# Kernel tuning notes

Measured on AMD Instinct MI355X. Metric: run time of the kernel, lower is better.

The kernel has to match this reference:

```python
import jax, jax.numpy as jnp
import numpy as np

B, L, E = 64, 256, 256
H, M, HD, R, O = 512, 256, 64, 4, 1024
CI = E + R * HD          # controller input size = 512
TO = H + R * HD          # pre-output size = 768
EPS = 1e-5


def _ln(x, g, b):
    m = jnp.mean(x, axis=-1, keepdims=True)
    v = jnp.mean((x - m) ** 2, axis=-1, keepdims=True)
    return (x - m) * jax.lax.rsqrt(v + EPS) * g + b


def setup_inputs() -> dict:
    key = jax.random.key(0)
    ks = jax.random.split(key, 12)
    s = 0.02
    return {
        "x_emb": jax.random.normal(ks[0], (B, L, E), jnp.float32),
        "W_ih": jax.random.normal(ks[1], (4 * H, CI), jnp.float32) * s,
        "W_hh": jax.random.normal(ks[2], (4 * H, H), jnp.float32) * s,
        "b_ih": jnp.zeros((4 * H,), jnp.float32),
        "b_hh": jnp.zeros((4 * H,), jnp.float32),
        "ln_in_g": jnp.ones((CI,), jnp.float32), "ln_in_b": jnp.zeros((CI,), jnp.float32),
        "ln_h_g": jnp.ones((H,), jnp.float32), "ln_h_b": jnp.zeros((H,), jnp.float32),
        "W_rk": jax.random.normal(ks[3], (R * HD, H), jnp.float32) * s, "b_rk": jnp.zeros((R * HD,), jnp.float32),
        "W_wk": jax.random.normal(ks[4], (HD, H), jnp.float32) * s, "b_wk": jnp.zeros((HD,), jnp.float32),
        "W_ws": jax.random.normal(ks[5], (1, H), jnp.float32) * s, "b_ws": jnp.zeros((1,), jnp.float32),
        "W_er": jax.random.normal(ks[6], (HD, H), jnp.float32) * s, "b_er": jnp.zeros((HD,), jnp.float32),
        "W_ad": jax.random.normal(ks[7], (HD, H), jnp.float32) * s, "b_ad": jnp.zeros((HD,), jnp.float32),
        "ln_rk_g": jnp.ones((HD,), jnp.float32), "ln_rk_b": jnp.zeros((HD,), jnp.float32),
        "ln_wk_g": jnp.ones((HD,), jnp.float32), "ln_wk_b": jnp.zeros((HD,), jnp.float32),
        "ln_mem_g": jnp.ones((HD,), jnp.float32), "ln_mem_b": jnp.zeros((HD,), jnp.float32),
        "ln_out_g": jnp.ones((TO,), jnp.float32), "ln_out_b": jnp.zeros((TO,), jnp.float32),
        "W_proj": jax.random.normal(ks[8], (O, TO), jnp.float32) * s, "b_proj": jnp.zeros((O,), jnp.float32),
    }


def reference(x_emb, W_ih, W_hh, b_ih, b_hh, ln_in_g, ln_in_b, ln_h_g, ln_h_b,
              W_rk, b_rk, W_wk, b_wk, W_ws, b_ws, W_er, b_er, W_ad, b_ad,
              ln_rk_g, ln_rk_b, ln_wk_g, ln_wk_b, ln_mem_g, ln_mem_b,
              ln_out_g, ln_out_b, W_proj, b_proj):
    Bd = x_emb.shape[0]

    def step(carry, x_t):
        h, c, memory, read_vec = carry
        ci = _ln(jnp.concatenate([x_t, read_vec], axis=-1), ln_in_g, ln_in_b)
        # single-step LSTM (PyTorch gate order i, f, g, o)
        gates = ci @ W_ih.T + h @ W_hh.T + b_ih + b_hh
        i, f, g, o = jnp.split(gates, 4, axis=-1)
        c = jax.nn.sigmoid(f) * c + jax.nn.sigmoid(i) * jnp.tanh(g)
        h = jax.nn.sigmoid(o) * jnp.tanh(c)
        hn = _ln(h, ln_h_g, ln_h_b)
        read_keys = (hn @ W_rk.T + b_rk).reshape(Bd, R, HD)
        write_keys = hn @ W_wk.T + b_wk                       # [B, HD]
        write_str = jax.nn.sigmoid(hn @ W_ws.T + b_ws)        # [B, 1]
        erase_vec = jax.nn.sigmoid(hn @ W_er.T + b_er)        # [B, HD]
        write_vec = jnp.tanh(hn @ W_ad.T + b_ad)              # [B, HD]
        # write
        mem_n = _ln(memory, ln_mem_g, ln_mem_b)
        wk = _ln(write_keys, ln_wk_g, ln_wk_b)
        ww = jax.nn.softmax(jnp.einsum('bh,bmh->bm', wk, mem_n), axis=1) * write_str  # [B, M]
        memory = memory * (1.0 - ww[:, :, None] * erase_vec[:, None, :]) + ww[:, :, None] * write_vec[:, None, :]
        # read
        mem_n2 = _ln(memory, ln_mem_g, ln_mem_b)
        rk = _ln(read_keys, ln_rk_g, ln_rk_b)
        rw = jax.nn.softmax(jnp.einsum('bnh,bmh->bnm', rk, mem_n2), axis=2)
        read_vec = jnp.einsum('bnm,bmh->bnh', rw, memory).reshape(Bd, R * HD)
        out = _ln(jnp.concatenate([hn, read_vec], axis=-1), ln_out_g, ln_out_b)
        logits = out @ W_proj.T + b_proj
        return (h, c, memory, read_vec), logits

    h0 = jnp.zeros((Bd, H), x_emb.dtype)
    c0 = jnp.zeros((Bd, H), x_emb.dtype)
    mem0 = jnp.zeros((Bd, M, HD), x_emb.dtype)
    rv0 = jnp.zeros((Bd, R * HD), x_emb.dtype)
    (h, c, memory, _), ys = jax.lax.scan(step, (h0, c0, mem0, rv0), jnp.swapaxes(x_emb, 0, 1))
    outputs = jnp.swapaxes(ys, 0, 1)  # [B, L, O]
    return outputs, memory, (h[None], c[None])
```

## Files before the change

kernel.cpp:

```cpp
#include <hip/hip_runtime.h>
#include <stdint.h>

#define Bn 64
#define Ln 256
#define En 256
#define Hn 512
#define Mn 256
#define HDn 64
#define Rn 4
#define On 1024
#define CIn 512
#define TOn 768
#define TB 1024
#define MP 65

typedef __attribute__((ext_vector_type(2))) _Float16 h2_t;

__device__ __forceinline__ float dot2(uint32_t a, uint32_t b, float c) {
  return __builtin_amdgcn_fdot2(__builtin_bit_cast(h2_t, a),
                                __builtin_bit_cast(h2_t, b), c, false);
}
__device__ __forceinline__ uint32_t pk2(float a, float b) {
  h2_t h; h.x = (_Float16)a; h.y = (_Float16)b;
  return __builtin_bit_cast(uint32_t, h);
}
__device__ __forceinline__ float sigm(float x) {
  float e = __expf(-fabsf(x)); float s = 1.0f / (1.0f + e);
  return x >= 0.0f ? s : 1.0f - s;
}
__device__ __forceinline__ float tanh_(float x) {
  float e = __expf(-2.0f * fabsf(x)); float t = (1.0f - e) / (1.0f + e);
  return x >= 0.0f ? t : -t;
}
__device__ __forceinline__ float ln64(float v, float g, float b) {
  float s = v;
  #pragma unroll
  for (int o = 32; o; o >>= 1) s += __shfl_xor(s, o);
  float mean = s * (1.f / 64.f);
  float d = v - mean; float q = d * d;
  #pragma unroll
  for (int o = 32; o; o >>= 1) q += __shfl_xor(q, o);
  float rstd = rsqrtf(q * (1.f / 64.f) + 1e-5f);
  return d * rstd * g + b;
}

__global__ void pack_gates4(const float* __restrict__ W_ih,
                            const float* __restrict__ W_hh,
                            uint4* __restrict__ Wg4) {
  int idx = blockIdx.x * 256 + threadIdx.x;
  if (idx >= 512 * 512) return;
  int kk = idx >> 9, u = idx & 511;
  int c = 2 * kk;
  float v[8];
  #pragma unroll
  for (int r = 0; r < 4; r++) {
    int row = r * 512 + u;
    float a, bb;
    if (c < 512) { a = W_ih[row * 512 + c];        bb = W_ih[row * 512 + c + 1]; }
    else         { a = W_hh[row * 512 + (c - 512)]; bb = W_hh[row * 512 + (c - 512) + 1]; }
    v[2 * r] = a; v[2 * r + 1] = bb;
  }
  uint4 w; w.x = pk2(v[0], v[1]); w.y = pk2(v[2], v[3]);
  w.z = pk2(v[4], v[5]); w.w = pk2(v[6], v[7]);
  Wg4[(size_t)kk * 512 + u] = w;
}

__global__ void pack_heads4(const float* __restrict__ W_rk, const float* __restrict__ W_wk,
                            const float* __restrict__ W_ws, const float* __restrict__ W_er,
                            const float* __restrict__ W_ad, uint4* __restrict__ Whd4) {
  int idx = blockIdx.x * 256 + threadIdx.x;
  if (idx >= 256 * 128) return;
  int kk = idx >> 7, s4 = idx & 127;
  int c = 2 * kk;
  float v[8];
  #pragma unroll
  for (int j = 0; j < 4; j++) {
    int s = 4 * s4 + j;
    float a = 0.f, bb = 0.f;
    if (s < 256)      { a = W_rk[s * 512 + c];          bb = W_rk[s * 512 + c + 1]; }
    else if (s < 320) { a = W_wk[(s - 256) * 512 + c];  bb = W_wk[(s - 256) * 512 + c + 1]; }
    else if (s == 320){ a = W_ws[c];                    bb = W_ws[c + 1]; }
    else if (s < 385) { a = W_er[(s - 321) * 512 + c];  bb = W_er[(s - 321) * 512 + c + 1]; }
    else if (s < 449) { a = W_ad[(s - 385) * 512 + c];  bb = W_ad[(s - 385) * 512 + c + 1]; }
    v[2 * j] = a; v[2 * j + 1] = bb;
  }
  uint4 w; w.x = pk2(v[0], v[1]); w.y = pk2(v[2], v[3]);
  w.z = pk2(v[4], v[5]); w.w = pk2(v[6], v[7]);
  Whd4[(size_t)kk * 128 + s4] = w;
}

__global__ void pack_proj(const float* __restrict__ W_proj, uint32_t* __restrict__ Wp) {
  int idx = blockIdx.x * blockDim.x + threadIdx.x;
  if (idx >= 1024 * 384) return;
  int o = idx / 384, kk = idx - o * 384;
  int c = 2 * kk;
  Wp[(size_t)kk * 1024 + o] = pk2(W_proj[o * 768 + c], W_proj[o * 768 + c + 1]);
}

struct Params {
  const float *x, *b_ih, *b_hh;
  const float *ln_in_g, *ln_in_b, *ln_h_g, *ln_h_b;
  const float *b_rk, *b_wk, *b_ws, *b_er, *b_ad;
  const float *ln_rk_g, *ln_rk_b, *ln_wk_g, *ln_wk_b;
  const float *ln_mem_g, *ln_mem_b, *ln_out_g, *ln_out_b;
  const uint4* Wg4; const uint4* Whd4;
  uint32_t* out16; float* out;
};

#define SMEM_FLOATS 32736
#define SMEM_BYTES  (SMEM_FLOATS * 4)

__global__ __launch_bounds__(TB, 1) void dnc_recur(Params p) {
  extern __shared__ float smem[];
  float* mem  = smem;
  float* h32  = mem + 16640;
  float* c32  = h32 + 512;
  float* hn32 = c32 + 512;
  float* rv32 = hn32 + 512;
  float* cvec = rv32 + 256;
  float* hd   = cvec + 512;
  float* wkn  = hd + 512;
  float* rkn  = wkn + 64;
  float* erv  = rkn + 256;
  float* wvv  = erv + 64;
  float* wsc  = wvv + 64;
  float* rsc  = wsc + 256;
  float* redA = rsc + 1024;
  float* redB = redA + 32;
  float* redC = redB + 32;
  float* redD = redC + 16;
  float* redE = redD + 32;
  float* misc = redE + 32;
  float* gpart= misc + 16;
  float* Lin_g= gpart + 4096;
  float* Lin_b= Lin_g + 512;
  float* Lh_g = Lin_b + 512;
  float* Lh_b = Lh_g + 512;
  float* Lo_g = Lh_b + 512;
  float* Lo_b = Lo_g + 768;
  float* Lrk_g= Lo_b + 768;
  float* Lrk_b= Lrk_g + 64;
  float* Lwk_g= Lrk_b + 64;
  float* Lwk_b= Lwk_g + 64;
  float* Lm_g = Lwk_b + 64;
  float* Lm_b = Lm_g + 64;
  float* bsum = Lm_b + 64;
  float* bhd  = bsum + 2048;
  uint32_t* act16 = (uint32_t*)(bhd + 512);
  uint32_t* hn16  = act16 + 512;

  const int tid = threadIdx.x;
  const int b = blockIdx.x;

  for (int i = tid; i < 16640; i += TB) mem[i] = 0.f;
  if (tid < 512) {
    h32[tid] = 0.f; c32[tid] = 0.f;
    Lin_g[tid] = p.ln_in_g[tid]; Lin_b[tid] = p.ln_in_b[tid];
    Lh_g[tid]  = p.ln_h_g[tid];  Lh_b[tid]  = p.ln_h_b[tid];
    float4 bs;
    bs.x = p.b_ih[tid]        + p.b_hh[tid];
    bs.y = p.b_ih[512 + tid]  + p.b_hh[512 + tid];
    bs.z = p.b_ih[1024 + tid] + p.b_hh[1024 + tid];
    bs.w = p.b_ih[1536 + tid] + p.b_hh[1536 + tid];
    ((float4*)bsum)[tid] = bs;
    float bb = 0.f;
    if (tid < 256)       bb = p.b_rk[tid];
    else if (tid < 320)  bb = p.b_wk[tid - 256];
    else if (tid == 320) bb = p.b_ws[0];
    else if (tid < 385)  bb = p.b_er[tid - 321];
    else if (tid < 449)  bb = p.b_ad[tid - 385];
    bhd[tid] = bb;
  }
  if (tid < 768) { Lo_g[tid] = p.ln_out_g[tid]; Lo_b[tid] = p.ln_out_b[tid]; }
  if (tid < 64) {
    Lrk_g[tid] = p.ln_rk_g[tid]; Lrk_b[tid] = p.ln_rk_b[tid];
    Lwk_g[tid] = p.ln_wk_g[tid]; Lwk_b[tid] = p.ln_wk_b[tid];
    Lm_g[tid]  = p.ln_mem_g[tid]; Lm_b[tid] = p.ln_mem_b[tid];
  }
  if (tid < 256) { rv32[tid] = 0.f; act16[256 + tid] = 0u; }
  __syncthreads();

  for (int t = 0; t < Ln; ++t) {
    if (tid < 256)      cvec[tid] = p.x[((size_t)b * Ln + t) * En + tid];
    else if (tid < 512) cvec[tid] = rv32[tid - 256];
    __syncthreads();
    {
      float v = (tid < 512) ? cvec[tid] : 0.f;
      float s = v, q = v * v;
      #pragma unroll
      for (int o = 32; o; o >>= 1) { s += __shfl_xor(s, o); q += __shfl_xor(q, o); }
      if ((tid & 63) == 0) { redA[tid >> 6] = s; redA[16 + (tid >> 6)] = q; }
    }
    __syncthreads();
    {
      float s = 0.f, q = 0.f;
      #pragma unroll
      for (int i = 0; i < 16; i++) { s += redA[i]; q += redA[16 + i]; }
      float mean = s * (1.f / 512.f);
      float rstd = rsqrtf(q * (1.f / 512.f) - mean * mean + 1e-5f);
      if (tid < 256) {
        float v0 = (cvec[2 * tid]     - mean) * rstd * Lin_g[2 * tid]     + Lin_b[2 * tid];
        float v1 = (cvec[2 * tid + 1] - mean) * rstd * Lin_g[2 * tid + 1] + Lin_b[2 * tid + 1];
        act16[tid] = pk2(v0, v1);
      }
    }
    __syncthreads();

    {
      int u = tid & 511, kh = tid >> 9;
      const uint4* wp = p.Wg4 + (size_t)(kh * 256) * 512 + u;
      const uint32_t* ap = act16 + kh * 256;
      float a0 = 0.f, a1 = 0.f, a2 = 0.f, a3 = 0.f;
      uint4 Ab[8], Bb[8];
      #pragma unroll
      for (int j = 0; j < 8; j++) Ab[j] = wp[(size_t)j * 512];
      #pragma unroll 1
      for (int c = 0; c < 32; c += 2) {
        #pragma unroll
        for (int j = 0; j < 8; j++) Bb[j] = wp[(size_t)((c + 1) * 8 + j) * 512];
        #pragma unroll
        for (int j = 0; j < 8; j++) {
          uint32_t a = ap[c * 8 + j];
          a0 = dot2(Ab[j].x, a, a0); a1 = dot2(Ab[j].y, a, a1);
          a2 = dot2(Ab[j].z, a, a2); a3 = dot2(Ab[j].w, a, a3);
        }
        int cn = (c + 2) & 31;
        #pragma unroll
        for (int j = 0; j < 8; j++) Ab[j] = wp[(size_t)(cn * 8 + j) * 512];
        #pragma unroll
        for (int j = 0; j < 8; j++) {
          uint32_t a = ap[(c + 1) * 8 + j];
          a0 = dot2(Bb[j].x, a, a0); a1 = dot2(Bb[j].y, a, a1);
          a2 = dot2(Bb[j].z, a, a2); a3 = dot2(Bb[j].w, a, a3);
        }
      }
      float4 r; r.x = a0; r.y = a1; r.z = a2; r.w = a3;
      ((float4*)(gpart + kh * 2048))[u] = r;
    }
    __syncthreads();

    if (tid < 512) {
      float4 pa = ((float4*)gpart)[tid];
      float4 pb = ((float4*)gpart)[512 + tid];
      float4 bs = ((float4*)bsum)[tid];
      float gi = pa.x + pb.x + bs.x;
      float gf = pa.y + pb.y + bs.y;
      float gg = pa.z + pb.z + bs.z;
      float go = pa.w + pb.w + bs.w;
      float c_ = sigm(gf) * c32[tid] + sigm(gi) * tanh_(gg);
      float h_ = sigm(go) * tanh_(c_);
      c32[tid] = c_; h32[tid] = h_;
    }
    __syncthreads();
    {
      float v = (tid < 512) ? h32[tid] : 0.f;
      float s = v, q = v * v;
      #pragma unroll
      for (int o = 32; o; o >>= 1) { s += __shfl_xor(s, o); q += __shfl_xor(q, o); }
      if ((tid & 63) == 0) { redB[tid >> 6] = s; redB[16 + (tid >> 6)] = q; }
    }
    __syncthreads();
    {
      float s = 0.f, q = 0.f;
      #pragma unroll
      for (int i = 0; i < 16; i++) { s += redB[i]; q += redB[16 + i]; }
      float mean = s * (1.f / Hn);
      float rstd = rsqrtf(q * (1.f / Hn) - mean * mean + 1e-5f);
      if (tid < 512) hn32[tid] = (h32[tid] - mean) * rstd * Lh_g[tid] + Lh_b[tid];
      if (tid < 256) {
        float v0 = (h32[2 * tid]     - mean) * rstd * Lh_g[2 * tid]     + Lh_b[2 * tid];
        float v1 = (h32[2 * tid + 1] - mean) * rstd * Lh_g[2 * tid + 1] + Lh_b[2 * tid + 1];
        hn16[tid] = pk2(v0, v1);
        act16[256 + tid] = pk2(h32[2 * tid], h32[2 * tid + 1]);
      }
    }
    __syncthreads();

    {
      int s4 = tid & 127, kp = tid >> 7;
      const uint4* wp = p.Whd4 + (size_t)(kp * 32) * 128 + s4;
      const uint32_t* ap = hn16 + kp * 32;
      float a0 = 0.f, a1 = 0.f, a2 = 0.f, a3 = 0.f;
      uint4 Ab[8], Bb[8];
      #pragma unroll
      for (int j = 0; j < 8; j++) Ab[j] = wp[(size_t)j * 128];
      #pragma unroll 1
      for (int c = 0; c < 4; c += 2) {
        #pragma unroll
        for (int j = 0; j < 8; j++) Bb[j] = wp[(size_t)((c + 1) * 8 + j) * 128];
        #pragma unroll
        for (int j = 0; j < 8; j++) {
          uint32_t a = ap[c * 8 + j];
          a0 = dot2(Ab[j].x, a, a0); a1 = dot2(Ab[j].y, a, a1);
          a2 = dot2(Ab[j].z, a, a2); a3 = dot2(Ab[j].w, a, a3);
        }
        int cn = (c + 2) & 3;
        #pragma unroll
        for (int j = 0; j < 8; j++) Ab[j] = wp[(size_t)(cn * 8 + j) * 128];
        #pragma unroll
        for (int j = 0; j < 8; j++) {
          uint32_t a = ap[(c + 1) * 8 + j];
          a0 = dot2(Bb[j].x, a, a0); a1 = dot2(Bb[j].y, a, a1);
          a2 = dot2(Bb[j].z, a, a2); a3 = dot2(Bb[j].w, a, a3);
        }
      }
      float4 r; r.x = a0; r.y = a1; r.z = a2; r.w = a3;
      ((float4*)(gpart + kp * 512))[s4] = r;
    }
    __syncthreads();
    if (tid < 512) {
      float acc = bhd[tid];
      #pragma unroll
      for (int kp = 0; kp < 8; kp++) acc += gpart[kp * 512 + tid];
      hd[tid] = acc;
    }
    __syncthreads();

    {
      int wid = tid >> 6, lane = tid & 63;
      if (wid == 0) {
        wkn[lane] = ln64(hd[256 + lane], Lwk_g[lane], Lwk_b[lane]);
      } else if (wid <= 4) {
        int n = wid - 1;
        rkn[n * 64 + lane] = ln64(hd[n * 64 + lane], Lrk_g[lane], Lrk_b[lane]);
      } else if (wid == 5) {
        erv[lane] = sigm(hd[321 + lane]);
      } else if (wid == 6) {
        wvv[lane] = tanh_(hd[385 + lane]);
      } else if (wid == 7 && lane == 0) {
        misc[0] = sigm(hd[320]);
      }
    }
    __syncthreads();

    {
      int m = tid >> 2, q = tid & 3;
      const float* mrow = mem + m * MP + q * 16;
      float s1 = 0.f, s2 = 0.f;
      #pragma unroll
      for (int j = 0; j < 16; j++) { float v = mrow[j]; s1 += v; s2 += v * v; }
      s1 += __shfl_xor(s1, 1); s1 += __shfl_xor(s1, 2);
      s2 += __shfl_xor(s2, 1); s2 += __shfl_xor(s2, 2);
      float mean = s1 * (1.f / 64.f);
      float rstd = rsqrtf(s2 * (1.f / 64.f) - mean * mean + 1e-5f);
      float d = 0.f;
      #pragma unroll
      for (int j = 0; j < 16; j++) {
        int jj = q * 16 + j;
        float mn = (mrow[j] - mean) * rstd * Lm_g[jj] + Lm_b[jj];
        d += wkn[jj] * mn;
      }
      d += __shfl_xor(d, 1); d += __shfl_xor(d, 2);
      if (q == 0) wsc[m] = d;
    }
    __syncthreads();
    float wsv = 0.f;
    if (tid < 256) {
      wsv = wsc[tid];
      float mx = wsv;
      #pragma unroll
      for (int o = 32; o; o >>= 1) mx = fmaxf(mx, __shfl_xor(mx, o));
      float e = __expf(wsv - mx);
      float sm = e;
      #pragma unroll
      for (int o = 32; o; o >>= 1) sm += __shfl_xor(sm, o);
      if ((tid & 63) == 0) { redC[tid >> 6] = mx; redC[8 + (tid >> 6)] = sm; }
    }
    __syncthreads();
    if (tid < 256) {
      float M = fmaxf(fmaxf(redC[0], redC[1]), fmaxf(redC[2], redC[3]));
      float S = redC[8]  * __expf(redC[0] - M) + redC[9]  * __expf(redC[1] - M)
              + redC[10] * __expf(redC[2] - M) + redC[11] * __expf(redC[3] - M);
      wsc[tid] = __expf(wsv - M) / S * misc[0];
    }
    __syncthreads();

    {
      int m = tid >> 2, q = tid & 3;
      float w = wsc[m];
      float* mrow = mem + m * MP + q * 16;
      float vals[16];
      float s1 = 0.f, s2 = 0.f;
      #pragma unroll
      for (int j = 0; j < 16; j++) {
        int jj = q * 16 + j;
        float v = mrow[j];
        v = v * (1.f - w * erv[jj]) + w * wvv[jj];
        mrow[j] = v;
        vals[j] = v;
        s1 += v; s2 += v * v;
      }
      s1 += __shfl_xor(s1, 1); s1 += __shfl_xor(s1, 2);
      s2 += __shfl_xor(s2, 1); s2 += __shfl_xor(s2, 2);
      float mean = s1 * (1.f / 64.f);
      float rstd = rsqrtf(s2 * (1.f / 64.f) - mean * mean + 1e-5f);
      float d0 = 0.f, d1 = 0.f, d2 = 0.f, d3 = 0.f;
      #pragma unroll
      for (int j = 0; j < 16; j++) {
        int jj = q * 16 + j;
        float mn = (vals[j] - mean) * rstd * Lm_g[jj] + Lm_b[jj];
        d0 += rkn[jj] * mn;       d1 += rkn[64 + jj] * mn;
        d2 += rkn[128 + jj] * mn; d3 += rkn[192 + jj] * mn;
      }
      d0 += __shfl_xor(d0, 1); d0 += __shfl_xor(d0, 2);
      d1 += __shfl_xor(d1, 1); d1 += __shfl_xor(d1, 2);
      d2 += __shfl_xor(d2, 1); d2 += __shfl_xor(d2, 2);
      d3 += __shfl_xor(d3, 1); d3 += __shfl_xor(d3, 2);
      if (q == 0) { rsc[m] = d0; rsc[256 + m] = d1; rsc[512 + m] = d2; rsc[768 + m] = d3; }
    }
    __syncthreads();
    float rsv;
    {
      int w = tid >> 6;
      rsv = rsc[tid];
      float mx = rsv;
      #pragma unroll
      for (int o = 32; o; o >>= 1) mx = fmaxf(mx, __shfl_xor(mx, o));
      float e = __expf(rsv - mx);
      float sm = e;
      #pragma unroll
      for (int o = 32; o; o >>= 1) sm += __shfl_xor(sm, o);
      if ((tid & 63) == 0) { redD[w] = mx; redD[16 + w] = sm; }
    }
    __syncthreads();
    {
      int n = tid >> 8;
      float M = fmaxf(fmaxf(redD[4 * n], redD[4 * n + 1]),
                      fmaxf(redD[4 * n + 2], redD[4 * n + 3]));
      float S = redD[16 + 4 * n]     * __expf(redD[4 * n]     - M)
              + redD[16 + 4 * n + 1] * __expf(redD[4 * n + 1] - M)
              + redD[16 + 4 * n + 2] * __expf(redD[4 * n + 2] - M)
              + redD[16 + 4 * n + 3] * __expf(redD[4 * n + 3] - M);
      rsc[tid] = __expf(rsv - M) / S;
    }
    __syncthreads();

    {
      int out = tid >> 2, q = tid & 3;
      int n = out >> 6, j = out & 63;
      const float* rw = rsc + n * 256 + q * 64;
      float acc = 0.f;
      #pragma unroll 8
      for (int mm = 0; mm < 64; ++mm)
        acc += rw[mm] * mem[(q * 64 + mm) * MP + j];
      acc += __shfl_xor(acc, 1); acc += __shfl_xor(acc, 2);
      if (q == 0) rv32[out] = acc;
    }
    __syncthreads();

    {
      float v = (tid < 512) ? hn32[tid] : (tid < 768 ? rv32[tid - 512] : 0.f);
      float s = v, q = v * v;
      #pragma unroll
      for (int o = 32; o; o >>= 1) { s += __shfl_xor(s, o); q += __shfl_xor(q, o); }
      if ((tid & 63) == 0) { redE[tid >> 6] = s; redE[16 + (tid >> 6)] = q; }
    }
    __syncthreads();
    {
      float s = 0.f, q = 0.f;
      #pragma unroll
      for (int i = 0; i < 16; i++) { s += redE[i]; q += redE[16 + i]; }
      float mean = s * (1.f / TOn);
      float rstd = rsqrtf(q * (1.f / TOn) - mean * mean + 1e-5f);
      if (tid < 384) {
        int e0 = 2 * tid, e1 = e0 + 1;
        float u0 = (e0 < 512) ? hn32[e0] : rv32[e0 - 512];
        float u1 = (e1 < 512) ? hn32[e1] : rv32[e1 - 512];
        u0 = (u0 - mean) * rstd * Lo_g[e0] + Lo_b[e0];
        u1 = (u1 - mean) * rstd * Lo_g[e1] + Lo_b[e1];
        p.out16[((size_t)b * Ln + t) * 384 + tid] = pk2(u0, u1);
      }
    }
  }

  const size_t OUT0 = (size_t)Bn * Ln * On;
  const size_t OUT1 = OUT0 + (size_t)Bn * Mn * HDn;
  const size_t OUT2 = OUT1 + (size_t)Bn * Hn;
  for (int i = tid; i < Mn * HDn; i += TB)
    p.out[OUT0 + (size_t)b * Mn * HDn + i] = mem[(i >> 6) * MP + (i & 63)];
  if (tid < Hn) {
    p.out[OUT1 + (size_t)b * Hn + tid] = h32[tid];
    p.out[OUT2 + (size_t)b * Hn + tid] = c32[tid];
  }
}

#define PROJ_ROWS 32
__global__ __launch_bounds__(1024, 1) void proj_gemm(const uint32_t* __restrict__ out16,
                                                     const uint32_t* __restrict__ Wp,
                                                     const float* __restrict__ b_proj,
                                                     float* __restrict__ out) {
  __shared__ uint32_t arow[PROJ_ROWS][384];
  int r0 = blockIdx.x * PROJ_ROWS;
  int tid = threadIdx.x;
  for (int i = tid; i < PROJ_ROWS * 384; i += 1024)
    ((uint32_t*)arow)[i] = out16[(size_t)r0 * 384 + i];
  __syncthreads();
  int cq = tid & 255, rg = tid >> 8;
  float acc[8][4];
  #pragma unroll
  for (int i = 0; i < 8; i++)
    #pragma unroll
    for (int j = 0; j < 4; j++) acc[i][j] = 0.f;
  for (int kk = 0; kk < 384; ++kk) {
    uint32_t w0 = Wp[(size_t)kk * 1024 + cq];
    uint32_t w1 = Wp[(size_t)kk * 1024 + cq + 256];
    uint32_t w2 = Wp[(size_t)kk * 1024 + cq + 512];
    uint32_t w3 = Wp[(size_t)kk * 1024 + cq + 768];
    #pragma unroll
    for (int i = 0; i < 8; i++) {
      uint32_t a = arow[rg * 8 + i][kk];
      acc[i][0] = dot2(w0, a, acc[i][0]); acc[i][1] = dot2(w1, a, acc[i][1]);
      acc[i][2] = dot2(w2, a, acc[i][2]); acc[i][3] = dot2(w3, a, acc[i][3]);
    }
  }
  #pragma unroll
  for (int i = 0; i < 8; i++) {
    size_t row = (size_t)r0 + rg * 8 + i;
    #pragma unroll
    for (int j = 0; j < 4; j++) {
      int c = cq + j * 256;
      out[row * 1024 + c] = acc[i][j] + b_proj[c];
    }
  }
}

static const size_t WS_WG    = 0;
static const size_t WS_WHD   = WS_WG  + (size_t)512 * 512 * 16;
static const size_t WS_WPJ   = WS_WHD + (size_t)256 * 128 * 16;
static const size_t WS_OUT16 = WS_WPJ + (size_t)384 * 1024 * 4;

extern "C" void kernel_launch(void* const* d_in, const int* in_sizes, int n_in,
                              void* d_out, int out_size, void* d_ws, size_t ws_size,
                              hipStream_t stream) {
  (void)in_sizes; (void)n_in; (void)out_size; (void)ws_size;
  const float* x       = (const float*)d_in[0];
  const float* W_ih    = (const float*)d_in[1];
  const float* W_hh    = (const float*)d_in[2];
  const float* b_ih    = (const float*)d_in[3];
  const float* b_hh    = (const float*)d_in[4];
  const float* ln_in_g = (const float*)d_in[5];
  const float* ln_in_b = (const float*)d_in[6];
  const float* ln_h_g  = (const float*)d_in[7];
  const float* ln_h_b  = (const float*)d_in[8];
  const float* W_rk    = (const float*)d_in[9];
  const float* b_rk    = (const float*)d_in[10];
  const float* W_wk    = (const float*)d_in[11];
  const float* b_wk    = (const float*)d_in[12];
  const float* W_ws    = (const float*)d_in[13];
  const float* b_ws    = (const float*)d_in[14];
  const float* W_er    = (const float*)d_in[15];
  const float* b_er    = (const float*)d_in[16];
  const float* W_ad    = (const float*)d_in[17];
  const float* b_ad    = (const float*)d_in[18];
  const float* ln_rk_g = (const float*)d_in[19];
  const float* ln_rk_b = (const float*)d_in[20];
  const float* ln_wk_g = (const float*)d_in[21];
  const float* ln_wk_b = (const float*)d_in[22];
  const float* ln_mem_g= (const float*)d_in[23];
  const float* ln_mem_b= (const float*)d_in[24];
  const float* ln_out_g= (const float*)d_in[25];
  const float* ln_out_b= (const float*)d_in[26];
  const float* W_proj  = (const float*)d_in[27];
  const float* b_proj  = (const float*)d_in[28];

  char* ws = (char*)d_ws;
  uint4*    Wg4   = (uint4*)(ws + WS_WG);
  uint4*    Whd4  = (uint4*)(ws + WS_WHD);
  uint32_t* Wp    = (uint32_t*)(ws + WS_WPJ);
  uint32_t* out16 = (uint32_t*)(ws + WS_OUT16);

  hipLaunchKernelGGL(pack_gates4, dim3(1024), dim3(256), 0, stream, W_ih, W_hh, Wg4);
  hipLaunchKernelGGL(pack_heads4, dim3(128), dim3(256), 0, stream,
                     W_rk, W_wk, W_ws, W_er, W_ad, Whd4);
  hipLaunchKernelGGL(pack_proj, dim3(1536), dim3(256), 0, stream, W_proj, Wp);

  Params p;
  p.x = x; p.b_ih = b_ih; p.b_hh = b_hh;
  p.ln_in_g = ln_in_g; p.ln_in_b = ln_in_b; p.ln_h_g = ln_h_g; p.ln_h_b = ln_h_b;
  p.b_rk = b_rk; p.b_wk = b_wk; p.b_ws = b_ws; p.b_er = b_er; p.b_ad = b_ad;
  p.ln_rk_g = ln_rk_g; p.ln_rk_b = ln_rk_b; p.ln_wk_g = ln_wk_g; p.ln_wk_b = ln_wk_b;
  p.ln_mem_g = ln_mem_g; p.ln_mem_b = ln_mem_b; p.ln_out_g = ln_out_g; p.ln_out_b = ln_out_b;
  p.Wg4 = Wg4; p.Whd4 = Whd4; p.out16 = out16; p.out = (float*)d_out;

  hipLaunchKernelGGL(dnc_recur, dim3(Bn), dim3(TB), SMEM_BYTES, stream, p);
  hipLaunchKernelGGL(proj_gemm, dim3((Bn * Ln) / PROJ_ROWS), dim3(1024), 0, stream,
                     out16, Wp, b_proj, (float*)d_out);
}
```

Before: 18.57 ms.

## Split recurrent GEMVs across 128 blocks with grid-wide barriers per timestep

The per-batch recurrent kernel becomes a persistent 128-block kernel. All blocks share the gate and head matvecs, with weights transposed so each block owns a row slice across all 64 batch items, and the results are exchanged through global buffers. The first 64 blocks still run the per-batch memory, softmax and LayerNorm work. Each timestep now uses four software grid barriers built on atomics and spin waits. In return, every block reads only its slice of the gate weights instead of the whole matrix. The cost is global-memory round trips and barrier latency, plus reliance on all blocks being co-resident and a timeout break that could hide a barrier that never completes.

```diff
diff --git a/kernel.cpp b/kernel.cpp
--- a/kernel.cpp
+++ b/kernel.cpp
@@ -7,12 +7,11 @@
 #define Hn 512
 #define Mn 256
 #define HDn 64
-#define Rn 4
 #define On 1024
-#define CIn 512
 #define TOn 768
+#define MP 65
+#define NBLK 128
 #define TB 1024
-#define MP 65
 
 typedef __attribute__((ext_vector_type(2))) _Float16 h2_t;
 
@@ -43,52 +42,60 @@
   float rstd = rsqrtf(q * (1.f / 64.f) + 1e-5f);
   return d * rstd * g + b;
 }
-
-__global__ void pack_gates4(const float* __restrict__ W_ih,
-                            const float* __restrict__ W_hh,
-                            uint4* __restrict__ Wg4) {
+__device__ __forceinline__ void blkstats(float v, float* red, int tid, float& S, float& Q) {
+  float s = v, q = v * v;
+  #pragma unroll
+  for (int o = 32; o; o >>= 1) { s += __shfl_xor(s, o); q += __shfl_xor(q, o); }
+  __syncthreads();
+  if ((tid & 63) == 0) { red[tid >> 6] = s; red[16 + (tid >> 6)] = q; }
+  __syncthreads();
+  S = 0.f; Q = 0.f;
+  #pragma unroll
+  for (int i = 0; i < 16; i++) { S += red[i]; Q += red[16 + i]; }
+}
+
+__device__ __forceinline__ void gsync(unsigned* cnt, unsigned& nbar, int tid) {
+  __syncthreads();
+  if (tid == 0) {
+    __threadfence();
+    __hip_atomic_fetch_add(cnt, 1u, __ATOMIC_RELEASE, __HIP_MEMORY_SCOPE_AGENT);
+    nbar++;
+    const unsigned target = nbar * NBLK;
+    long long t0 = clock64();
+    while (__hip_atomic_load(cnt, __ATOMIC_ACQUIRE, __HIP_MEMORY_SCOPE_AGENT) < target) {
+      __builtin_amdgcn_s_sleep(1);
+      if (clock64() - t0 > 8000000LL) break;
+    }
+    __threadfence();
+  }
+  __syncthreads();
+}
+
+__global__ void pack_gT(const float* __restrict__ W_ih, const float* __restrict__ W_hh,
+                        uint32_t* __restrict__ WgT) {
   int idx = blockIdx.x * 256 + threadIdx.x;
-  if (idx >= 512 * 512) return;
-  int kk = idx >> 9, u = idx & 511;
+  if (idx >= 512 * 2048) return;
+  int kk = idx >> 11, row = idx & 2047;
+  float a, b;
+  if (kk < 256) { int c = 2 * kk;       a = W_ih[row * 512 + c]; b = W_ih[row * 512 + c + 1]; }
+  else          { int c = 2 * kk - 512; a = W_hh[row * 512 + c]; b = W_hh[row * 512 + c + 1]; }
+  WgT[idx] = pk2(a, b);
+}
+__global__ void pack_hT(const float* __restrict__ W_rk, const float* __restrict__ W_wk,
+                        const float* __restrict__ W_ws, const float* __restrict__ W_er,
+                        const float* __restrict__ W_ad, uint32_t* __restrict__ WhdT) {
+  int idx = blockIdx.x * 256 + threadIdx.x;
+  if (idx >= 256 * 512) return;
+  int kk = idx >> 9, s = idx & 511;
   int c = 2 * kk;
-  float v[8];
-  #pragma unroll
-  for (int r = 0; r < 4; r++) {
-    int row = r * 512 + u;
-    float a, bb;
-    if (c < 512) { a = W_ih[row * 512 + c];        bb = W_ih[row * 512 + c + 1]; }
-    else         { a = W_hh[row * 512 + (c - 512)]; bb = W_hh[row * 512 + (c - 512) + 1]; }
-    v[2 * r] = a; v[2 * r + 1] = bb;
-  }
-  uint4 w; w.x = pk2(v[0], v[1]); w.y = pk2(v[2], v[3]);
-  w.z = pk2(v[4], v[5]); w.w = pk2(v[6], v[7]);
-  Wg4[(size_t)kk * 512 + u] = w;
-}
-
-__global__ void pack_heads4(const float* __restrict__ W_rk, const float* __restrict__ W_wk,
-                            const float* __restrict__ W_ws, const float* __restrict__ W_er,
-                            const float* __restrict__ W_ad, uint4* __restrict__ Whd4) {
-  int idx = blockIdx.x * 256 + threadIdx.x;
-  if (idx >= 256 * 128) return;
-  int kk = idx >> 7, s4 = idx & 127;
-  int c = 2 * kk;
-  float v[8];
-  #pragma unroll
-  for (int j = 0; j < 4; j++) {
-    int s = 4 * s4 + j;
-    float a = 0.f, bb = 0.f;
-    if (s < 256)      { a = W_rk[s * 512 + c];          bb = W_rk[s * 512 + c + 1]; }
-    else if (s < 320) { a = W_wk[(s - 256) * 512 + c];  bb = W_wk[(s - 256) * 512 + c + 1]; }
-    else if (s == 320){ a = W_ws[c];                    bb = W_ws[c + 1]; }
-    else if (s < 385) { a = W_er[(s - 321) * 512 + c];  bb = W_er[(s - 321) * 512 + c + 1]; }
-    else if (s < 449) { a = W_ad[(s - 385) * 512 + c];  bb = W_ad[(s - 385) * 512 + c + 1]; }
-    v[2 * j] = a; v[2 * j + 1] = bb;
-  }
-  uint4 w; w.x = pk2(v[0], v[1]); w.y = pk2(v[2], v[3]);
-  w.z = pk2(v[4], v[5]); w.w = pk2(v[6], v[7]);
-  Whd4[(size_t)kk * 128 + s4] = w;
-}
-
+  float a = 0.f, b = 0.f;
+  if (s < 256)      { a = W_rk[s * 512 + c];          b = W_rk[s * 512 + c + 1]; }
+  else if (s < 320) { a = W_wk[(s - 256) * 512 + c];  b = W_wk[(s - 256) * 512 + c + 1]; }
+  else if (s == 320){ a = W_ws[c];                    b = W_ws[c + 1]; }
+  else if (s < 385) { a = W_er[(s - 321) * 512 + c];  b = W_er[(s - 321) * 512 + c + 1]; }
+  else if (s < 449) { a = W_ad[(s - 385) * 512 + c];  b = W_ad[(s - 385) * 512 + c + 1]; }
+  WhdT[idx] = pk2(a, b);
+}
 __global__ void pack_proj(const float* __restrict__ W_proj, uint32_t* __restrict__ Wp) {
   int idx = blockIdx.x * blockDim.x + threadIdx.x;
   if (idx >= 1024 * 384) return;
@@ -98,22 +105,26 @@
 }
 
 struct Params {
-  const float *x, *b_ih, *b_hh;
-  const float *ln_in_g, *ln_in_b, *ln_h_g, *ln_h_b;
+  const float* x;
+  const uint32_t *WgT, *WhdT;
+  uint32_t *actT, *hnT;
+  float *gates, *heads;
+  unsigned* sync;
+  uint32_t* out16; float* out;
+  const float *b_ih, *b_hh, *ln_in_g, *ln_in_b, *ln_h_g, *ln_h_b;
   const float *b_rk, *b_wk, *b_ws, *b_er, *b_ad;
-  const float *ln_rk_g, *ln_rk_b, *ln_wk_g, *ln_wk_b;
-  const float *ln_mem_g, *ln_mem_b, *ln_out_g, *ln_out_b;
-  const uint4* Wg4; const uint4* Whd4;
-  uint32_t* out16; float* out;
+  const float *ln_rk_g, *ln_rk_b, *ln_wk_g, *ln_wk_b, *ln_mem_g, *ln_mem_b;
+  const float *ln_out_g, *ln_out_b;
 };
 
-#define SMEM_FLOATS 32736
+#define SMEM_FLOATS 36256
 #define SMEM_BYTES  (SMEM_FLOATS * 4)
 
-__global__ __launch_bounds__(TB, 1) void dnc_recur(Params p) {
+__global__ __launch_bounds__(TB, 1) void dnc_step(Params p) {
   extern __shared__ float smem[];
   float* mem  = smem;
-  float* h32  = mem + 16640;
+  float* slab = mem + 16640;
+  float* h32  = slab + 8448;
   float* c32  = h32 + 512;
   float* hn32 = c32 + 512;
   float* rv32 = hn32 + 512;
@@ -126,361 +137,352 @@
   float* wsc  = wvv + 64;
   float* rsc  = wsc + 256;
   float* redA = rsc + 1024;
-  float* redB = redA + 32;
-  float* redC = redB + 32;
+  float* redC = redA + 32;
   float* redD = redC + 16;
-  float* redE = redD + 32;
-  float* misc = redE + 32;
-  float* gpart= misc + 16;
-  float* Lin_g= gpart + 4096;
-  float* Lin_b= Lin_g + 512;
-  float* Lh_g = Lin_b + 512;
-  float* Lh_b = Lh_g + 512;
-  float* Lo_g = Lh_b + 512;
-  float* Lo_b = Lo_g + 768;
-  float* Lrk_g= Lo_b + 768;
-  float* Lrk_b= Lrk_g + 64;
-  float* Lwk_g= Lrk_b + 64;
-  float* Lwk_b= Lwk_g + 64;
-  float* Lm_g = Lwk_b + 64;
-  float* Lm_b = Lm_g + 64;
-  float* bsum = Lm_b + 64;
+  float* misc = redD + 32;
+  float* bsum = misc + 16;
   float* bhd  = bsum + 2048;
-  uint32_t* act16 = (uint32_t*)(bhd + 512);
-  uint32_t* hn16  = act16 + 512;
-
-  const int tid = threadIdx.x;
-  const int b = blockIdx.x;
-
-  for (int i = tid; i < 16640; i += TB) mem[i] = 0.f;
-  if (tid < 512) {
-    h32[tid] = 0.f; c32[tid] = 0.f;
-    Lin_g[tid] = p.ln_in_g[tid]; Lin_b[tid] = p.ln_in_b[tid];
-    Lh_g[tid]  = p.ln_h_g[tid];  Lh_b[tid]  = p.ln_h_b[tid];
-    float4 bs;
-    bs.x = p.b_ih[tid]        + p.b_hh[tid];
-    bs.y = p.b_ih[512 + tid]  + p.b_hh[512 + tid];
-    bs.z = p.b_ih[1024 + tid] + p.b_hh[1024 + tid];
-    bs.w = p.b_ih[1536 + tid] + p.b_hh[1536 + tid];
-    ((float4*)bsum)[tid] = bs;
-    float bb = 0.f;
-    if (tid < 256)       bb = p.b_rk[tid];
-    else if (tid < 320)  bb = p.b_wk[tid - 256];
-    else if (tid == 320) bb = p.b_ws[0];
-    else if (tid < 385)  bb = p.b_er[tid - 321];
-    else if (tid < 449)  bb = p.b_ad[tid - 385];
-    bhd[tid] = bb;
-  }
-  if (tid < 768) { Lo_g[tid] = p.ln_out_g[tid]; Lo_b[tid] = p.ln_out_b[tid]; }
-  if (tid < 64) {
-    Lrk_g[tid] = p.ln_rk_g[tid]; Lrk_b[tid] = p.ln_rk_b[tid];
-    Lwk_g[tid] = p.ln_wk_g[tid]; Lwk_b[tid] = p.ln_wk_b[tid];
-    Lm_g[tid]  = p.ln_mem_g[tid]; Lm_b[tid] = p.ln_mem_b[tid];
-  }
-  if (tid < 256) { rv32[tid] = 0.f; act16[256 + tid] = 0u; }
-  __syncthreads();
-
-  for (int t = 0; t < Ln; ++t) {
-    if (tid < 256)      cvec[tid] = p.x[((size_t)b * Ln + t) * En + tid];
-    else if (tid < 512) cvec[tid] = rv32[tid - 256];
+  float* Lin_g = bhd + 512;
+  float* Lin_b = Lin_g + 512;
+  float* Lh_g  = Lin_b + 512;
+  float* Lh_b  = Lh_g + 512;
+  float* Lo_g  = Lh_b + 512;
+  float* Lo_b  = Lo_g + 768;
+  float* Lrk_g = Lo_b + 768;
+  float* Lrk_b = Lrk_g + 64;
+  float* Lwk_g = Lrk_b + 64;
+  float* Lwk_b = Lwk_g + 64;
+  float* Lm_g  = Lwk_b + 64;
+  float* Lm_b  = Lm_g + 64;
+
+  const int tid  = threadIdx.x;
+  const int bid  = blockIdx.x;
+  const int lane = tid & 63;
+  const int wv   = tid >> 6;
+  const bool master = (bid < 64);
+  const int b = bid;
+  unsigned nbar = 0;
+
+  if (master) {
+    for (int i = tid; i < 16640; i += TB) mem[i] = 0.f;
+    if (tid < 512) {
+      h32[tid] = 0.f; c32[tid] = 0.f;
+      Lin_g[tid] = p.ln_in_g[tid]; Lin_b[tid] = p.ln_in_b[tid];
+      Lh_g[tid]  = p.ln_h_g[tid];  Lh_b[tid]  = p.ln_h_b[tid];
+      float4 bs;
+      bs.x = p.b_ih[tid]        + p.b_hh[tid];
+      bs.y = p.b_ih[512 + tid]  + p.b_hh[512 + tid];
+      bs.z = p.b_ih[1024 + tid] + p.b_hh[1024 + tid];
+      bs.w = p.b_ih[1536 + tid] + p.b_hh[1536 + tid];
+      ((float4*)bsum)[tid] = bs;
+      float bb = 0.f;
+      if (tid < 256)       bb = p.b_rk[tid];
+      else if (tid < 320)  bb = p.b_wk[tid - 256];
+      else if (tid == 320) bb = p.b_ws[0];
+      else if (tid < 385)  bb = p.b_er[tid - 321];
+      else if (tid < 449)  bb = p.b_ad[tid - 385];
+      bhd[tid] = bb;
+    }
+    if (tid < 768) { Lo_g[tid] = p.ln_out_g[tid]; Lo_b[tid] = p.ln_out_b[tid]; }
+    if (tid < 64) {
+      Lrk_g[tid] = p.ln_rk_g[tid]; Lrk_b[tid] = p.ln_rk_b[tid];
+      Lwk_g[tid] = p.ln_wk_g[tid]; Lwk_b[tid] = p.ln_wk_b[tid];
+      Lm_g[tid]  = p.ln_mem_g[tid]; Lm_b[tid] = p.ln_mem_b[tid];
+    }
+    if (tid < 256) rv32[tid] = 0.f;
+    __syncthreads();
+    if (tid < 256)      cvec[tid] = p.x[(size_t)b * 65536 + tid];
+    else if (tid < 512) cvec[tid] = 0.f;
     __syncthreads();
     {
       float v = (tid < 512) ? cvec[tid] : 0.f;
-      float s = v, q = v * v;
-      #pragma unroll
-      for (int o = 32; o; o >>= 1) { s += __shfl_xor(s, o); q += __shfl_xor(q, o); }
-      if ((tid & 63) == 0) { redA[tid >> 6] = s; redA[16 + (tid >> 6)] = q; }
-    }
-    __syncthreads();
-    {
-      float s = 0.f, q = 0.f;
-      #pragma unroll
-      for (int i = 0; i < 16; i++) { s += redA[i]; q += redA[16 + i]; }
-      float mean = s * (1.f / 512.f);
-      float rstd = rsqrtf(q * (1.f / 512.f) - mean * mean + 1e-5f);
+      float S, Q; blkstats(v, redA, tid, S, Q);
+      float mean = S * (1.f / 512.f);
+      float rstd = rsqrtf(Q * (1.f / 512.f) - mean * mean + 1e-5f);
       if (tid < 256) {
         float v0 = (cvec[2 * tid]     - mean) * rstd * Lin_g[2 * tid]     + Lin_b[2 * tid];
         float v1 = (cvec[2 * tid + 1] - mean) * rstd * Lin_g[2 * tid + 1] + Lin_b[2 * tid + 1];
-        act16[tid] = pk2(v0, v1);
-      }
-    }
-    __syncthreads();
-
+        p.actT[tid * 64 + b] = pk2(v0, v1);
+      } else if (tid < 512) {
+        p.actT[tid * 64 + b] = 0u;
+      }
+    }
+  }
+  gsync(p.sync, nbar, tid);
+
+  for (int t = 0; t < Ln; ++t) {
     {
-      int u = tid & 511, kh = tid >> 9;
-      const uint4* wp = p.Wg4 + (size_t)(kh * 256) * 512 + u;
-      const uint32_t* ap = act16 + kh * 256;
+      const int R0 = bid * 16;
+      float acc[16];
+      #pragma unroll
+      for (int i = 0; i < 16; i++) acc[i] = 0.f;
+      const int kk0 = wv * 32;
+      for (int kk = kk0; kk < kk0 + 32; ++kk) {
+        uint32_t a = p.actT[kk * 64 + lane];
+        const uint32_t* wr = p.WgT + (size_t)kk * 2048 + R0;
+        uint4 w0 = *(const uint4*)(wr);
+        uint4 w1 = *(const uint4*)(wr + 4);
+        uint4 w2 = *(const uint4*)(wr + 8);
+        uint4 w3 = *(const uint4*)(wr + 12);
+        acc[0]  = dot2(w0.x, a, acc[0]);  acc[1]  = dot2(w0.y, a, acc[1]);
+        acc[2]  = dot2(w0.z, a, acc[2]);  acc[3]  = dot2(w0.w, a, acc[3]);
+        acc[4]  = dot2(w1.x, a, acc[4]);  acc[5]  = dot2(w1.y, a, acc[5]);
+        acc[6]  = dot2(w1.z, a, acc[6]);  acc[7]  = dot2(w1.w, a, acc[7]);
+        acc[8]  = dot2(w2.x, a, acc[8]);  acc[9]  = dot2(w2.y, a, acc[9]);
+        acc[10] = dot2(w2.z, a, acc[10]); acc[11] = dot2(w2.w, a, acc[11]);
+        acc[12] = dot2(w3.x, a, acc[12]); acc[13] = dot2(w3.y, a, acc[13]);
+        acc[14] = dot2(w3.z, a, acc[14]); acc[15] = dot2(w3.w, a, acc[15]);
+      }
+      const int q = wv & 7;
+      if (wv < 8) {
+        #pragma unroll
+        for (int r = 0; r < 16; r++) slab[q * 1056 + r * 66 + lane] = acc[r];
+      }
+      __syncthreads();
+      if (wv >= 8) {
+        #pragma unroll
+        for (int r = 0; r < 16; r++) slab[q * 1056 + r * 66 + lane] += acc[r];
+      }
+      __syncthreads();
+      {
+        int r = wv, bb = lane;
+        float s = 0.f;
+        #pragma unroll
+        for (int q2 = 0; q2 < 8; q2++) s += slab[q2 * 1056 + r * 66 + bb];
+        p.gates[(size_t)(R0 + r) * 64 + bb] = s;
+      }
+    }
+    gsync(p.sync, nbar, tid);
+
+    if (master) {
+      if (tid < 512) {
+        float4 bs = ((float4*)bsum)[tid];
+        float gi = p.gates[(size_t)tid * 64 + b]          + bs.x;
+        float gf = p.gates[(size_t)(512 + tid) * 64 + b]  + bs.y;
+        float gg = p.gates[(size_t)(1024 + tid) * 64 + b] + bs.z;
+        float go = p.gates[(size_t)(1536 + tid) * 64 + b] + bs.w;
+        float c_ = sigm(gf) * c32[tid] + sigm(gi) * tanh_(gg);
+        float h_ = sigm(go) * tanh_(c_);
+        c32[tid] = c_; h32[tid] = h_;
+      }
+      __syncthreads();
+      {
+        float v = (tid < 512) ? h32[tid] : 0.f;
+        float S, Q; blkstats(v, redA, tid, S, Q);
+        float mean = S * (1.f / Hn);
+        float rstd = rsqrtf(Q * (1.f / Hn) - mean * mean + 1e-5f);
+        if (tid < 512) hn32[tid] = (h32[tid] - mean) * rstd * Lh_g[tid] + Lh_b[tid];
+      }
+      __syncthreads();
+      if (tid < 256) p.hnT[tid * 64 + b] = pk2(hn32[2 * tid], hn32[2 * tid + 1]);
+    }
+    gsync(p.sync, nbar, tid);
+
+    {
+      const int S0s = bid * 4;
       float a0 = 0.f, a1 = 0.f, a2 = 0.f, a3 = 0.f;
-      uint4 Ab[8], Bb[8];
-      #pragma unroll
-      for (int j = 0; j < 8; j++) Ab[j] = wp[(size_t)j * 512];
-      #pragma unroll 1
-      for (int c = 0; c < 32; c += 2) {
-        #pragma unroll
-        for (int j = 0; j < 8; j++) Bb[j] = wp[(size_t)((c + 1) * 8 + j) * 512];
-        #pragma unroll
-        for (int j = 0; j < 8; j++) {
-          uint32_t a = ap[c * 8 + j];
-          a0 = dot2(Ab[j].x, a, a0); a1 = dot2(Ab[j].y, a, a1);
-          a2 = dot2(Ab[j].z, a, a2); a3 = dot2(Ab[j].w, a, a3);
+      const int kk0 = wv * 16;
+      for (int kk = kk0; kk < kk0 + 16; ++kk) {
+        uint32_t a = p.hnT[kk * 64 + lane];
+        uint4 w = *(const uint4*)(p.WhdT + (size_t)kk * 512 + S0s);
+        a0 = dot2(w.x, a, a0); a1 = dot2(w.y, a, a1);
+        a2 = dot2(w.z, a, a2); a3 = dot2(w.w, a, a3);
+      }
+      const int q = wv & 7;
+      if (wv < 8) {
+        slab[q * 264 + lane]       = a0; slab[q * 264 + 66 + lane]  = a1;
+        slab[q * 264 + 132 + lane] = a2; slab[q * 264 + 198 + lane] = a3;
+      }
+      __syncthreads();
+      if (wv >= 8) {
+        slab[q * 264 + lane]       += a0; slab[q * 264 + 66 + lane]  += a1;
+        slab[q * 264 + 132 + lane] += a2; slab[q * 264 + 198 + lane] += a3;
+      }
+      __syncthreads();
+      if (tid < 256) {
+        int s = tid >> 6, bb = tid & 63;
+        float sum = 0.f;
+        #pragma unroll
+        for (int q2 = 0; q2 < 8; q2++) sum += slab[q2 * 264 + s * 66 + bb];
+        p.heads[(size_t)(S0s + s) * 64 + bb] = sum;
+      }
+    }
+    gsync(p.sync, nbar, tid);
+
+    if (master) {
+      if (tid < 512) hd[tid] = p.heads[(size_t)tid * 64 + b] + bhd[tid];
+      __syncthreads();
+      {
+        int wid = wv, ln = lane;
+        if (wid == 0) {
+          wkn[ln] = ln64(hd[256 + ln], Lwk_g[ln], Lwk_b[ln]);
+        } else if (wid <= 4) {
+          int n = wid - 1;
+          rkn[n * 64 + ln] = ln64(hd[n * 64 + ln], Lrk_g[ln], Lrk_b[ln]);
+        } else if (wid == 5) {
+          erv[ln] = sigm(hd[321 + ln]);
+        } else if (wid == 6) {
+          wvv[ln] = tanh_(hd[385 + ln]);
+        } else if (wid == 7 && ln == 0) {
+          misc[0] = sigm(hd[320]);
         }
-        int cn = (c + 2) & 31;
-        #pragma unroll
-        for (int j = 0; j < 8; j++) Ab[j] = wp[(size_t)(cn * 8 + j) * 512];
-        #pragma unroll
-        for (int j = 0; j < 8; j++) {
-          uint32_t a = ap[(c + 1) * 8 + j];
-          a0 = dot2(Bb[j].x, a, a0); a1 = dot2(Bb[j].y, a, a1);
-          a2 = dot2(Bb[j].z, a, a2); a3 = dot2(Bb[j].w, a, a3);
+      }
+      __syncthreads();
+      {
+        int m = tid >> 2, q = tid & 3;
+        const float* mrow = mem + m * MP + q * 16;
+        float s1 = 0.f, s2 = 0.f;
+        #pragma unroll
+        for (int j = 0; j < 16; j++) { float v = mrow[j]; s1 += v; s2 += v * v; }
+        s1 += __shfl_xor(s1, 1); s1 += __shfl_xor(s1, 2);
+        s2 += __shfl_xor(s2, 1); s2 += __shfl_xor(s2, 2);
+        float mean = s1 * (1.f / 64.f);
+        float rstd = rsqrtf(s2 * (1.f / 64.f) - mean * mean + 1e-5f);
+        float d = 0.f;
+        #pragma unroll
+        for (int j = 0; j < 16; j++) {
+          int jj = q * 16 + j;
+          float mn = (mrow[j] - mean) * rstd * Lm_g[jj] + Lm_b[jj];
+          d += wkn[jj] * mn;
         }
-      }
-      float4 r; r.x = a0; r.y = a1; r.z = a2; r.w = a3;
-      ((float4*)(gpart + kh * 2048))[u] = r;
-    }
-    __syncthreads();
-
-    if (tid < 512) {
-      float4 pa = ((float4*)gpart)[tid];
-      float4 pb = ((float4*)gpart)[512 + tid];
-      float4 bs = ((float4*)bsum)[tid];
-      float gi = pa.x + pb.x + bs.x;
-      float gf = pa.y + pb.y + bs.y;
-      float gg = pa.z + pb.z + bs.z;
-      float go = pa.w + pb.w + bs.w;
-      float c_ = sigm(gf) * c32[tid] + sigm(gi) * tanh_(gg);
-      float h_ = sigm(go) * tanh_(c_);
-      c32[tid] = c_; h32[tid] = h_;
-    }
-    __syncthreads();
-    {
-      float v = (tid < 512) ? h32[tid] : 0.f;
-      float s = v, q = v * v;
-      #pragma unroll
-      for (int o = 32; o; o >>= 1) { s += __shfl_xor(s, o); q += __shfl_xor(q, o); }
-      if ((tid & 63) == 0) { redB[tid >> 6] = s; redB[16 + (tid >> 6)] = q; }
-    }
-    __syncthreads();
-    {
-      float s = 0.f, q = 0.f;
-      #pragma unroll
-      for (int i = 0; i < 16; i++) { s += redB[i]; q += redB[16 + i]; }
-      float mean = s * (1.f / Hn);
-      float rstd = rsqrtf(q * (1.f / Hn) - mean * mean + 1e-5f);
-      if (tid < 512) hn32[tid] = (h32[tid] - mean) * rstd * Lh_g[tid] + Lh_b[tid];
+        d += __shfl_xor(d, 1); d += __shfl_xor(d, 2);
+        if (q == 0) wsc[m] = d;
+      }
+      __syncthreads();
+      float wsv = 0.f;
       if (tid < 256) {
-        float v0 = (h32[2 * tid]     - mean) * rstd * Lh_g[2 * tid]     + Lh_b[2 * tid];
-        float v1 = (h32[2 * tid + 1] - mean) * rstd * Lh_g[2 * tid + 1] + Lh_b[2 * tid + 1];
-        hn16[tid] = pk2(v0, v1);
-        act16[256 + tid] = pk2(h32[2 * tid], h32[2 * tid + 1]);
-      }
-    }
-    __syncthreads();
-
-    {
-      int s4 = tid & 127, kp = tid >> 7;
-      const uint4* wp = p.Whd4 + (size_t)(kp * 32) * 128 + s4;
-      const uint32_t* ap = hn16 + kp * 32;
-      float a0 = 0.f, a1 = 0.f, a2 = 0.f, a3 = 0.f;
-      uint4 Ab[8], Bb[8];
-      #pragma unroll
-      for (int j = 0; j < 8; j++) Ab[j] = wp[(size_t)j * 128];
-      #pragma unroll 1
-      for (int c = 0; c < 4; c += 2) {
-        #pragma unroll
-        for (int j = 0; j < 8; j++) Bb[j] = wp[(size_t)((c + 1) * 8 + j) * 128];
-        #pragma unroll
-        for (int j = 0; j < 8; j++) {
-          uint32_t a = ap[c * 8 + j];
-          a0 = dot2(Ab[j].x, a, a0); a1 = dot2(Ab[j].y, a, a1);
-          a2 = dot2(Ab[j].z, a, a2); a3 = dot2(Ab[j].w, a, a3);
+        wsv = wsc[tid];
+        float mx = wsv;
+        #pragma unroll
+        for (int o = 32; o; o >>= 1) mx = fmaxf(mx, __shfl_xor(mx, o));
+        float e = __expf(wsv - mx);
+        float sm = e;
+        #pragma unroll
+        for (int o = 32; o; o >>= 1) sm += __shfl_xor(sm, o);
+        if ((tid & 63) == 0) { redC[tid >> 6] = mx; redC[8 + (tid >> 6)] = sm; }
+      }
+      __syncthreads();
+      if (tid < 256) {
+        float M = fmaxf(fmaxf(redC[0], redC[1]), fmaxf(redC[2], redC[3]));
+        float S = redC[8]  * __expf(redC[0] - M) + redC[9]  * __expf(redC[1] - M)
+                + redC[10] * __expf(redC[2] - M) + redC[11] * __expf(redC[3] - M);
+        wsc[tid] = __expf(wsv - M) / S * misc[0];
+      }
+      __syncthreads();
+      {
+        int m = tid >> 2, q = tid & 3;
+        float w = wsc[m];
+        float* mrow = mem + m * MP + q * 16;
+        float vals[16];
+        float s1 = 0.f, s2 = 0.f;
+        #pragma unroll
+        for (int j = 0; j < 16; j++) {
+          int jj = q * 16 + j;
+          float v = mrow[j];
+          v = v * (1.f - w * erv[jj]) + w * wvv[jj];
+          mrow[j] = v; vals[j] = v;
+          s1 += v; s2 += v * v;
         }
-        int cn = (c + 2) & 3;
-        #pragma unroll
-        for (int j = 0; j < 8; j++) Ab[j] = wp[(size_t)(cn * 8 + j) * 128];
-        #pragma unroll
-        for (int j = 0; j < 8; j++) {
-          uint32_t a = ap[(c + 1) * 8 + j];
-          a0 = dot2(Bb[j].x, a, a0); a1 = dot2(Bb[j].y, a, a1);
-          a2 = dot2(Bb[j].z, a, a2); a3 = dot2(Bb[j].w, a, a3);
+        s1 += __shfl_xor(s1, 1); s1 += __shfl_xor(s1, 2);
+        s2 += __shfl_xor(s2, 1); s2 += __shfl_xor(s2, 2);
+        float mean = s1 * (1.f / 64.f);
+        float rstd = rsqrtf(s2 * (1.f / 64.f) - mean * mean + 1e-5f);
+        float d0 = 0.f, d1 = 0.f, d2 = 0.f, d3 = 0.f;
+        #pragma unroll
+        for (int j = 0; j < 16; j++) {
+          int jj = q * 16 + j;
+          float mn = (vals[j] - mean) * rstd * Lm_g[jj] + Lm_b[jj];
+          d0 += rkn[jj] * mn;       d1 += rkn[64 + jj] * mn;
+          d2 += rkn[128 + jj] * mn; d3 += rkn[192 + jj] * mn;
         }
-      }
-      float4 r; r.x = a0; r.y = a1; r.z = a2; r.w = a3;
-      ((float4*)(gpart + kp * 512))[s4] = r;
-    }
-    __syncthreads();
-    if (tid < 512) {
-      float acc = bhd[tid];
-      #pragma unroll
-      for (int kp = 0; kp < 8; kp++) acc += gpart[kp * 512 + tid];
-      hd[tid] = acc;
-    }
-    __syncthreads();
-
-    {
-      int wid = tid >> 6, lane = tid & 63;
-      if (wid == 0) {
-        wkn[lane] = ln64(hd[256 + lane], Lwk_g[lane], Lwk_b[lane]);
-      } else if (wid <= 4) {
-        int n = wid - 1;
-        rkn[n * 64 + lane] = ln64(hd[n * 64 + lane], Lrk_g[lane], Lrk_b[lane]);
-      } else if (wid == 5) {
-        erv[lane] = sigm(hd[321 + lane]);
-      } else if (wid == 6) {
-        wvv[lane] = tanh_(hd[385 + lane]);
-      } else if (wid == 7 && lane == 0) {
-        misc[0] = sigm(hd[320]);
-      }
-    }
-    __syncthreads();
-
-    {
-      int m = tid >> 2, q = tid & 3;
-      const float* mrow = mem + m * MP + q * 16;
-      float s1 = 0.f, s2 = 0.f;
-      #pragma unroll
-      for (int j = 0; j < 16; j++) { float v = mrow[j]; s1 += v; s2 += v * v; }
-      s1 += __shfl_xor(s1, 1); s1 += __shfl_xor(s1, 2);
-      s2 += __shfl_xor(s2, 1); s2 += __shfl_xor(s2, 2);
-      float mean = s1 * (1.f / 64.f);
-      float rstd = rsqrtf(s2 * (1.f / 64.f) - mean * mean + 1e-5f);
-      float d = 0.f;
-      #pragma unroll
-      for (int j = 0; j < 16; j++) {
-        int jj = q * 16 + j;
-        float mn = (mrow[j] - mean) * rstd * Lm_g[jj] + Lm_b[jj];
-        d += wkn[jj] * mn;
-      }
-      d += __shfl_xor(d, 1); d += __shfl_xor(d, 2);
-      if (q == 0) wsc[m] = d;
-    }
-    __syncthreads();
-    float wsv = 0.f;
-    if (tid < 256) {
-      wsv = wsc[tid];
-      float mx = wsv;
-      #pragma unroll
-      for (int o = 32; o; o >>= 1) mx = fmaxf(mx, __shfl_xor(mx, o));
-      float e = __expf(wsv - mx);
-      float sm = e;
-      #pragma unroll
-      for (int o = 32; o; o >>= 1) sm += __shfl_xor(sm, o);
-      if ((tid & 63) == 0) { redC[tid >> 6] = mx; redC[8 + (tid >> 6)] = sm; }
-    }
-    __syncthreads();
-    if (tid < 256) {
-      float M = fmaxf(fmaxf(redC[0], redC[1]), fmaxf(redC[2], redC[3]));
-      float S = redC[8]  * __expf(redC[0] - M) + redC[9]  * __expf(redC[1] - M)
-              + redC[10] * __expf(redC[2] - M) + redC[11] * __expf(redC[3] - M);
-      wsc[tid] = __expf(wsv - M) / S * misc[0];
-    }
-    __syncthreads();
-
-    {
-      int m = tid >> 2, q = tid & 3;
-      float w = wsc[m];
-      float* mrow = mem + m * MP + q * 16;
-      float vals[16];
-      float s1 = 0.f, s2 = 0.f;
-      #pragma unroll
-      for (int j = 0; j < 16; j++) {
-        int jj = q * 16 + j;
-        float v = mrow[j];
-        v = v * (1.f - w * erv[jj]) + w * wvv[jj];
-        mrow[j] = v;
-        vals[j] = v;
-        s1 += v; s2 += v * v;
-      }
-      s1 += __shfl_xor(s1, 1); s1 += __shfl_xor(s1, 2);
-      s2 += __shfl_xor(s2, 1); s2 += __shfl_xor(s2, 2);
-      float mean = s1 * (1.f / 64.f);
-      float rstd = rsqrtf(s2 * (1.f / 64.f) - mean * mean + 1e-5f);
-      float d0 = 0.f, d1 = 0.f, d2 = 0.f, d3 = 0.f;
-      #pragma unroll
-      for (int j = 0; j < 16; j++) {
-        int jj = q * 16 + j;
-        float mn = (vals[j] - mean) * rstd * Lm_g[jj] + Lm_b[jj];
-        d0 += rkn[jj] * mn;       d1 += rkn[64 + jj] * mn;
-        d2 += rkn[128 + jj] * mn; d3 += rkn[192 + jj] * mn;
-      }
-      d0 += __shfl_xor(d0, 1); d0 += __shfl_xor(d0, 2);
-      d1 += __shfl_xor(d1, 1); d1 += __shfl_xor(d1, 2);
-      d2 += __shfl_xor(d2, 1); d2 += __shfl_xor(d2, 2);
-      d3 += __shfl_xor(d3, 1); d3 += __shfl_xor(d3, 2);
-      if (q == 0) { rsc[m] = d0; rsc[256 + m] = d1; rsc[512 + m] = d2; rsc[768 + m] = d3; }
-    }
-    __syncthreads();
-    float rsv;
-    {
-      int w = tid >> 6;
-      rsv = rsc[tid];
-      float mx = rsv;
-      #pragma unroll
-      for (int o = 32; o; o >>= 1) mx = fmaxf(mx, __shfl_xor(mx, o));
-      float e = __expf(rsv - mx);
-      float sm = e;
-      #pragma unroll
-      for (int o = 32; o; o >>= 1) sm += __shfl_xor(sm, o);
-      if ((tid & 63) == 0) { redD[w] = mx; redD[16 + w] = sm; }
-    }
-    __syncthreads();
-    {
-      int n = tid >> 8;
-      float M = fmaxf(fmaxf(redD[4 * n], redD[4 * n + 1]),
-                      fmaxf(redD[4 * n + 2], redD[4 * n + 3]));
-      float S = redD[16 + 4 * n]     * __expf(redD[4 * n]     - M)
-              + redD[16 + 4 * n + 1] * __expf(redD[4 * n + 1] - M)
-              + redD[16 + 4 * n + 2] * __expf(redD[4 * n + 2] - M)
-              + redD[16 + 4 * n + 3] * __expf(redD[4 * n + 3] - M);
-      rsc[tid] = __expf(rsv - M) / S;
-    }
-    __syncthreads();
-
-    {
-      int out = tid >> 2, q = tid & 3;
-      int n = out >> 6, j = out & 63;
-      const float* rw = rsc + n * 256 + q * 64;
-      float acc = 0.f;
-      #pragma unroll 8
-      for (int mm = 0; mm < 64; ++mm)
-        acc += rw[mm] * mem[(q * 64 + mm) * MP + j];
-      acc += __shfl_xor(acc, 1); acc += __shfl_xor(acc, 2);
-      if (q == 0) rv32[out] = acc;
-    }
-    __syncthreads();
-
-    {
-      float v = (tid < 512) ? hn32[tid] : (tid < 768 ? rv32[tid - 512] : 0.f);
-      float s = v, q = v * v;
-      #pragma unroll
-      for (int o = 32; o; o >>= 1) { s += __shfl_xor(s, o); q += __shfl_xor(q, o); }
-      if ((tid & 63) == 0) { redE[tid >> 6] = s; redE[16 + (tid >> 6)] = q; }
-    }
-    __syncthreads();
-    {
-      float s = 0.f, q = 0.f;
-      #pragma unroll
-      for (int i = 0; i < 16; i++) { s += redE[i]; q += redE[16 + i]; }
-      float mean = s * (1.f / TOn);
-      float rstd = rsqrtf(q * (1.f / TOn) - mean * mean + 1e-5f);
-      if (tid < 384) {
-        int e0 = 2 * tid, e1 = e0 + 1;
-        float u0 = (e0 < 512) ? hn32[e0] : rv32[e0 - 512];
-        float u1 = (e1 < 512) ? hn32[e1] : rv32[e1 - 512];
-        u0 = (u0 - mean) * rstd * Lo_g[e0] + Lo_b[e0];
-        u1 = (u1 - mean) * rstd * Lo_g[e1] + Lo_b[e1];
-        p.out16[((size_t)b * Ln + t) * 384 + tid] = pk2(u0, u1);
-      }
-    }
+        d0 += __shfl_xor(d0, 1); d0 += __shfl_xor(d0, 2);
+        d1 += __shfl_xor(d1, 1); d1 += __shfl_xor(d1, 2);
+        d2 += __shfl_xor(d2, 1); d2 += __shfl_xor(d2, 2);
+        d3 += __shfl_xor(d3, 1); d3 += __shfl_xor(d3, 2);
+        if (q == 0) { rsc[m] = d0; rsc[256 + m] = d1; rsc[512 + m] = d2; rsc[768 + m] = d3; }
+      }
+      __syncthreads();
+      float rsv;
+      {
+        rsv = rsc[tid];
+        float mx = rsv;
+        #pragma unroll
+        for (int o = 32; o; o >>= 1) mx = fmaxf(mx, __shfl_xor(mx, o));
+        float e = __expf(rsv - mx);
+        float sm = e;
+        #pragma unroll
+        for (int o = 32; o; o >>= 1) sm += __shfl_xor(sm, o);
+        if ((tid & 63) == 0) { redD[wv] = mx; redD[16 + wv] = sm; }
+      }
+      __syncthreads();
+      {
+        int n = tid >> 8;
+        float M = fmaxf(fmaxf(redD[4 * n], redD[4 * n + 1]),
+                        fmaxf(redD[4 * n + 2], redD[4 * n + 3]));
+        float S = redD[16 + 4 * n]     * __expf(redD[4 * n]     - M)
+                + redD[16 + 4 * n + 1] * __expf(redD[4 * n + 1] - M)
+                + redD[16 + 4 * n + 2] * __expf(redD[4 * n + 2] - M)
+                + redD[16 + 4 * n + 3] * __expf(redD[4 * n + 3] - M);
+        rsc[tid] = __expf(rsv - M) / S;
+      }
+      __syncthreads();
+      {
+        int out = tid >> 2, q = tid & 3;
+        int n = out >> 6, j = out & 63;
+        const float* rw = rsc + n * 256 + q * 64;
+        float acc = 0.f;
+        #pragma unroll 8
+        for (int mm = 0; mm < 64; ++mm)
+          acc += rw[mm] * mem[(q * 64 + mm) * MP + j];
+        acc += __shfl_xor(acc, 1); acc += __shfl_xor(acc, 2);
+        if (q == 0) rv32[out] = acc;
+      }
+      __syncthreads();
+      {
+        float v = (tid < 512) ? hn32[tid] : (tid < 768 ? rv32[tid - 512] : 0.f);
+        float S, Q; blkstats(v, redA, tid, S, Q);
+        float mean = S * (1.f / TOn);
+        float rstd = rsqrtf(Q * (1.f / TOn) - mean * mean + 1e-5f);
+        if (tid < 384) {
+          int e0 = 2 * tid, e1 = e0 + 1;
+          float u0 = (e0 < 512) ? hn32[e0] : rv32[e0 - 512];
+          float u1 = (e1 < 512) ? hn32[e1] : rv32[e1 - 512];
+          u0 = (u0 - mean) * rstd * Lo_g[e0] + Lo_b[e0];
+          u1 = (u1 - mean) * rstd * Lo_g[e1] + Lo_b[e1];
+          p.out16[((size_t)b * Ln + t) * 384 + tid] = pk2(u0, u1);
+        }
+      }
+      if (t < Ln - 1) {
+        if (tid < 256)      cvec[tid] = p.x[((size_t)b * Ln + (t + 1)) * En + tid];
+        else if (tid < 512) cvec[tid] = rv32[tid - 256];
+        __syncthreads();
+        float v = (tid < 512) ? cvec[tid] : 0.f;
+        float S, Q; blkstats(v, redA, tid, S, Q);
+        float mean = S * (1.f / 512.f);
+        float rstd = rsqrtf(Q * (1.f / 512.f) - mean * mean + 1e-5f);
+        if (tid < 256) {
+          float v0 = (cvec[2 * tid]     - mean) * rstd * Lin_g[2 * tid]     + Lin_b[2 * tid];
+          float v1 = (cvec[2 * tid + 1] - mean) * rstd * Lin_g[2 * tid + 1] + Lin_b[2 * tid + 1];
+          p.actT[tid * 64 + b] = pk2(v0, v1);
+        } else if (tid < 512) {
+          int k = tid - 256;
+          p.actT[tid * 64 + b] = pk2(h32[2 * k], h32[2 * k + 1]);
+        }
+      }
+    }
+    gsync(p.sync, nbar, tid);
   }
 
-  const size_t OUT0 = (size_t)Bn * Ln * On;
-  const size_t OUT1 = OUT0 + (size_t)Bn * Mn * HDn;
-  const size_t OUT2 = OUT1 + (size_t)Bn * Hn;
-  for (int i = tid; i < Mn * HDn; i += TB)
-    p.out[OUT0 + (size_t)b * Mn * HDn + i] = mem[(i >> 6) * MP + (i & 63)];
-  if (tid < Hn) {
-    p.out[OUT1 + (size_t)b * Hn + tid] = h32[tid];
-    p.out[OUT2 + (size_t)b * Hn + tid] = c32[tid];
+  if (master) {
+    const size_t OUT0 = (size_t)Bn * Ln * On;
+    const size_t OUT1 = OUT0 + (size_t)Bn * Mn * HDn;
+    const size_t OUT2 = OUT1 + (size_t)Bn * Hn;
+    for (int i = tid; i < Mn * HDn; i += TB)
+      p.out[OUT0 + (size_t)b * Mn * HDn + i] = mem[(i >> 6) * MP + (i & 63)];
+    if (tid < Hn) {
+      p.out[OUT1 + (size_t)b * Hn + tid] = h32[tid];
+      p.out[OUT2 + (size_t)b * Hn + tid] = c32[tid];
+    }
   }
 }
 
@@ -524,10 +526,15 @@
   }
 }
 
-static const size_t WS_WG    = 0;
-static const size_t WS_WHD   = WS_WG  + (size_t)512 * 512 * 16;
-static const size_t WS_WPJ   = WS_WHD + (size_t)256 * 128 * 16;
-static const size_t WS_OUT16 = WS_WPJ + (size_t)384 * 1024 * 4;
+static const size_t WS_WGT   = 0;
+static const size_t WS_WHDT  = WS_WGT   + (size_t)512 * 2048 * 4;
+static const size_t WS_WPJ   = WS_WHDT  + (size_t)256 * 512 * 4;
+static const size_t WS_ACTT  = WS_WPJ   + (size_t)384 * 1024 * 4;
+static const size_t WS_HNT   = WS_ACTT  + (size_t)512 * 64 * 4;
+static const size_t WS_GATES = WS_HNT   + (size_t)256 * 64 * 4;
+static const size_t WS_HEADS = WS_GATES + (size_t)2048 * 64 * 4;
+static const size_t WS_OUT16 = WS_HEADS + (size_t)512 * 64 * 4;
+static const size_t WS_SYNC  = WS_OUT16 + (size_t)16384 * 384 * 4;
 
 extern "C" void kernel_launch(void* const* d_in, const int* in_sizes, int n_in,
                               void* d_out, int out_size, void* d_ws, size_t ws_size,
@@ -564,25 +571,35 @@
   const float* b_proj  = (const float*)d_in[28];
 
   char* ws = (char*)d_ws;
-  uint4*    Wg4   = (uint4*)(ws + WS_WG);
-  uint4*    Whd4  = (uint4*)(ws + WS_WHD);
+  uint32_t* WgT   = (uint32_t*)(ws + WS_WGT);
+  uint32_t* WhdT  = (uint32_t*)(ws + WS_WHDT);
   uint32_t* Wp    = (uint32_t*)(ws + WS_WPJ);
+  uint32_t* actT  = (uint32_t*)(ws + WS_ACTT);
+  uint32_t* hnT   = (uint32_t*)(ws + WS_HNT);
+  float*    gates = (float*)(ws + WS_GATES);
+  float*    heads = (float*)(ws + WS_HEADS);
   uint32_t* out16 = (uint32_t*)(ws + WS_OUT16);
-
-  hipLaunchKernelGGL(pack_gates4, dim3(1024), dim3(256), 0, stream, W_ih, W_hh, Wg4);
-  hipLaunchKernelGGL(pack_heads4, dim3(128), dim3(256), 0, stream,
-                     W_rk, W_wk, W_ws, W_er, W_ad, Whd4);
+  unsigned* syncp = (unsigned*)(ws + WS_SYNC);
+
+  hipMemsetAsync(syncp, 0, 256, stream);
+
+  hipLaunchKernelGGL(pack_gT, dim3(4096), dim3(256), 0, stream, W_ih, W_hh, WgT);
+  hipLaunchKernelGGL(pack_hT, dim3(512), dim3(256), 0, stream,
+                     W_rk, W_wk, W_ws, W_er, W_ad, WhdT);
   hipLaunchKernelGGL(pack_proj, dim3(1536), dim3(256), 0, stream, W_proj, Wp);
 
   Params p;
-  p.x = x; p.b_ih = b_ih; p.b_hh = b_hh;
+  p.x = x; p.WgT = WgT; p.WhdT = WhdT;
+  p.actT = actT; p.hnT = hnT; p.gates = gates; p.heads = heads;
+  p.sync = syncp; p.out16 = out16; p.out = (float*)d_out;
+  p.b_ih = b_ih; p.b_hh = b_hh;
   p.ln_in_g = ln_in_g; p.ln_in_b = ln_in_b; p.ln_h_g = ln_h_g; p.ln_h_b = ln_h_b;
   p.b_rk = b_rk; p.b_wk = b_wk; p.b_ws = b_ws; p.b_er = b_er; p.b_ad = b_ad;
   p.ln_rk_g = ln_rk_g; p.ln_rk_b = ln_rk_b; p.ln_wk_g = ln_wk_g; p.ln_wk_b = ln_wk_b;
   p.ln_mem_g = ln_mem_g; p.ln_mem_b = ln_mem_b; p.ln_out_g = ln_out_g; p.ln_out_b = ln_out_b;
-  p.Wg4 = Wg4; p.Whd4 = Whd4; p.out16 = out16; p.out = (float*)d_out;
-
-  hipLaunchKernelGGL(dnc_recur, dim3(Bn), dim3(TB), SMEM_BYTES, stream, p);
+
+  hipLaunchKernelGGL(dnc_step, dim3(NBLK), dim3(TB), SMEM_BYTES, stream, p);
+
   hipLaunchKernelGGL(proj_gemm, dim3((Bn * Ln) / PROJ_ROWS), dim3(1024), 0, stream,
                      out16, Wp, b_proj, (float*)d_out);
 }
```

New measurement: 31.29 ms. 68.5% more time.
